# Optimization experiments

Measured on AMD Instinct MI355X. Metric: run time of the kernel, lower is better.

## Reference

```python
import jax, jax.numpy as jnp
import numpy as np

DIM = 128
BATCH = 1024


def _init_linear(key, fan_in, fan_out):
    kw, kb = jax.random.split(key)
    bound = 1.0 / np.sqrt(fan_in)
    W = jax.random.uniform(kw, (fan_in, fan_out), jnp.float32, -bound, bound)
    b = jax.random.uniform(kb, (fan_out,), jnp.float32, -bound, bound)
    return W, b


def setup_inputs() -> dict:
    key = jax.random.key(0)
    kx, ky, k1, k2, k3, k4 = jax.random.split(key, 6)
    x = jax.random.normal(kx, (BATCH, DIM), jnp.float32)
    y = jax.random.normal(ky, (BATCH, DIM), jnp.float32)
    W1, b1 = _init_linear(k1, 2 * DIM, 128)
    W2, b2 = _init_linear(k2, 128, 64)
    W3, b3 = _init_linear(k3, 64, 8)
    W4, b4 = _init_linear(k4, 8, 1)
    return {"x": x, "y": y, "W1": W1, "b1": b1, "W2": W2, "b2": b2,
            "W3": W3, "b3": b3, "W4": W4, "b4": b4}


def reference(x, y, W1, b1, W2, b2, W3, b3, W4, b4):
    # Original: pairs[i, j] = concat(x[j], y[i]); scores -> [B, B]; return transpose,
    # i.e. out[a, b] = f(concat(x[a], y[b])).
    # Split first linear algebraically: concat(x, y) @ W1 = x @ W1[:d] + y @ W1[d:].
    d = x.shape[1]
    xa = x @ W1[:d]          # [B, 128]
    yb = y @ W1[d:]          # [B, 128]
    h = jax.nn.relu(xa[:, None, :] + yb[None, :, :] + b1)  # [B, B, 128]
    h = jax.nn.relu(h @ W2 + b2)                            # [B, B, 64]
    h = jax.nn.relu(h @ W3 + b3)                            # [B, B, 8]
    out = (h @ W4 + b4)[..., 0]                             # [B, B]
    return out
```

## Files before the change

### kernel.cpp

```cpp
#include <hip/hip_runtime.h>
#include <hip/hip_bf16.h>

typedef float f32x4 __attribute__((ext_vector_type(4)));
typedef float f32x16 __attribute__((ext_vector_type(16)));
typedef short s16x8 __attribute__((ext_vector_type(8)));
typedef unsigned int u32x4 __attribute__((ext_vector_type(4)));

__device__ __forceinline__ short f2bf(float v) {
    __hip_bfloat16 h = __float2bfloat16(v);
    return __builtin_bit_cast(short, h);
}
__device__ __forceinline__ unsigned cvtpk(float lo, float hi) {
    unsigned r;
    asm("v_cvt_pk_bf16_f32 %0, %1, %2" : "=v"(r) : "v"(lo), "v"(hi));
    return r;
}
__device__ __forceinline__ void swap32(unsigned &x, unsigned &y) {
    asm("v_permlane32_swap_b32 %0, %1" : "+v"(x), "+v"(y));
}

__global__ __launch_bounds__(128) void precompute_kernel(
    const float* __restrict__ x, const float* __restrict__ y,
    const float* __restrict__ W1, const float* __restrict__ b1,
    float* __restrict__ xa, float* __restrict__ yb)
{
    __shared__ float rows[8][128];
    const int bid = blockIdx.x;
    const int k = threadIdx.x;
    const bool is_x = bid < 128;
    const int r0 = (is_x ? bid : bid - 128) * 8;
    const float* src = (is_x ? x : y) + (size_t)r0 * 128;
    const float* w = is_x ? W1 : (W1 + 128 * 128);
#pragma unroll
    for (int r = 0; r < 8; ++r) rows[r][k] = src[r * 128 + k];
    __syncthreads();
    float acc[8];
    const float bias = is_x ? b1[k] : 0.0f;
#pragma unroll
    for (int r = 0; r < 8; ++r) acc[r] = bias;
    for (int d = 0; d < 128; ++d) {
        float wv = w[d * 128 + k];
#pragma unroll
        for (int r = 0; r < 8; ++r) acc[r] = fmaf(rows[r][d], wv, acc[r]);
    }
    float* dst = (is_x ? xa : yb) + (size_t)r0 * 128 + k;
#pragma unroll
    for (int r = 0; r < 8; ++r) dst[r * 128] = acc[r];
}

__global__ __launch_bounds__(256, 2) void fused_kernel(
    const float* __restrict__ xa, const float* __restrict__ yb,
    const float* __restrict__ W2, const float* __restrict__ b2,
    const float* __restrict__ W3, const float* __restrict__ b3,
    const float* __restrict__ W4, const float* __restrict__ b4,
    float* __restrict__ out)
{
    __shared__ float xa_lds[16 * 128];

    const int tid = threadIdx.x;
    const int bid = blockIdx.x;
    const int a_chunk = bid >> 3;
    const int bq = bid & 7;
    const int wave = tid >> 6;
    const int lane = tid & 63;
    const int half = lane >> 5;
    const int m = lane & 31;
    const int bg = bq * 4 + wave;

    {
        const f32x4* xsrc = (const f32x4*)(xa + (size_t)a_chunk * 16 * 128);
        f32x4* dst = (f32x4*)xa_lds;
        dst[tid] = xsrc[tid];
        dst[tid + 256] = xsrc[tid + 256];
    }

    f32x4 yv0[8], yv1[8];
    {
        const float* yrow = yb + (size_t)(bg * 32 + m) * 128 + half * 8;
#pragma unroll
        for (int s = 0; s < 8; ++s) {
            yv0[s] = *(const f32x4*)&yrow[s * 16];
            yv1[s] = *(const f32x4*)&yrow[s * 16 + 4];
        }
    }

    s16x8 W2a[2][8];
#pragma unroll
    for (int mt = 0; mt < 2; ++mt)
#pragma unroll
        for (int s = 0; s < 8; ++s)
#pragma unroll
            for (int j = 0; j < 8; ++j)
                W2a[mt][s][j] = f2bf(W2[(s * 16 + half * 8 + j) * 64 + mt * 32 + m]);

    s16x8 W3a[4];
#pragma unroll
    for (int s = 0; s < 4; ++s)
#pragma unroll
        for (int j = 0; j < 8; ++j)
            W3a[s][j] = (m < 8) ? f2bf(W3[(s * 16 + half * 8 + j) * 8 + m]) : (short)0;

    f32x16 b2v0, b2v1, c3init;
#pragma unroll
    for (int r = 0; r < 16; ++r) {
        int f = (r & 3) + 8 * (r >> 2) + 4 * half;
        b2v0[r] = b2[f];
        b2v1[r] = b2[f + 32];
        c3init[r] = (r < 4) ? b3[(r & 3) + 4 * half] : 0.0f;
    }
    float w4v[4];
#pragma unroll
    for (int j = 0; j < 4; ++j) w4v[j] = W4[j + 4 * half];
    const float b4s = b4[0];

    __syncthreads();

    float* outp = out + (size_t)(a_chunk * 16) * 1024 + bg * 32 + m;

    for (int ai = 0; ai < 16; ++ai) {
        const float* xr = &xa_lds[ai * 128 + half * 8];
        f32x16 c20, c21;
#pragma unroll
        for (int s = 0; s < 8; ++s) {
            f32x4 x0 = *(const f32x4*)&xr[s * 16];
            f32x4 x1 = *(const f32x4*)&xr[s * 16 + 4];
            f32x4 h0 = x0 + yv0[s];
            f32x4 h1 = x1 + yv1[s];
            u32x4 q;
            q.x = cvtpk(fmaxf(h0.x, 0.f), fmaxf(h0.y, 0.f));
            q.y = cvtpk(fmaxf(h0.z, 0.f), fmaxf(h0.w, 0.f));
            q.z = cvtpk(fmaxf(h1.x, 0.f), fmaxf(h1.y, 0.f));
            q.w = cvtpk(fmaxf(h1.z, 0.f), fmaxf(h1.w, 0.f));
            s16x8 bfrag = __builtin_bit_cast(s16x8, q);
            if (s == 0) {
                c20 = __builtin_amdgcn_mfma_f32_32x32x16_bf16(W2a[0][0], bfrag, b2v0, 0, 0, 0);
                c21 = __builtin_amdgcn_mfma_f32_32x32x16_bf16(W2a[1][0], bfrag, b2v1, 0, 0, 0);
            } else {
                c20 = __builtin_amdgcn_mfma_f32_32x32x16_bf16(W2a[0][s], bfrag, c20, 0, 0, 0);
                c21 = __builtin_amdgcn_mfma_f32_32x32x16_bf16(W2a[1][s], bfrag, c21, 0, 0, 0);
            }
        }

        unsigned P[8], Q[8];
#pragma unroll
        for (int i = 0; i < 8; ++i) {
            P[i] = cvtpk(fmaxf(c20[2 * i], 0.f), fmaxf(c20[2 * i + 1], 0.f));
            Q[i] = cvtpk(fmaxf(c21[2 * i], 0.f), fmaxf(c21[2 * i + 1], 0.f));
        }
        s16x8 bf3[4];
        {
            unsigned w0 = P[0], w2 = P[2]; swap32(w0, w2);
            unsigned w1 = P[1], w3 = P[3]; swap32(w1, w3);
            u32x4 t; t.x = w0; t.y = w1; t.z = w2; t.w = w3;
            bf3[0] = __builtin_bit_cast(s16x8, t);
            unsigned v0 = P[4], v2 = P[6]; swap32(v0, v2);
            unsigned v1 = P[5], v3 = P[7]; swap32(v1, v3);
            u32x4 u; u.x = v0; u.y = v1; u.z = v2; u.w = v3;
            bf3[1] = __builtin_bit_cast(s16x8, u);
            unsigned a0 = Q[0], a2 = Q[2]; swap32(a0, a2);
            unsigned a1 = Q[1], a3 = Q[3]; swap32(a1, a3);
            u32x4 t2; t2.x = a0; t2.y = a1; t2.z = a2; t2.w = a3;
            bf3[2] = __builtin_bit_cast(s16x8, t2);
            unsigned e0 = Q[4], e2 = Q[6]; swap32(e0, e2);
            unsigned e1 = Q[5], e3 = Q[7]; swap32(e1, e3);
            u32x4 u2; u2.x = e0; u2.y = e1; u2.z = e2; u2.w = e3;
            bf3[3] = __builtin_bit_cast(s16x8, u2);
        }

        f32x16 c3 = __builtin_amdgcn_mfma_f32_32x32x16_bf16(W3a[0], bf3[0], c3init, 0, 0, 0);
#pragma unroll
        for (int s = 1; s < 4; ++s)
            c3 = __builtin_amdgcn_mfma_f32_32x32x16_bf16(W3a[s], bf3[s], c3, 0, 0, 0);

        float p = fmaxf(c3[0], 0.f) * w4v[0] + fmaxf(c3[1], 0.f) * w4v[1]
                + fmaxf(c3[2], 0.f) * w4v[2] + fmaxf(c3[3], 0.f) * w4v[3];
        unsigned pu = __builtin_bit_cast(unsigned, p);
        unsigned pv = pu;
        asm("" : "+v"(pv));
        swap32(pu, pv);
        float r = __builtin_bit_cast(float, pu) + __builtin_bit_cast(float, pv) + b4s;
        if (half == 0)
            outp[(size_t)ai * 1024] = r;
    }
}

extern "C" void kernel_launch(void* const* d_in, const int* in_sizes, int n_in,
                              void* d_out, int out_size, void* d_ws, size_t ws_size,
                              hipStream_t stream) {
    const float* x  = (const float*)d_in[0];
    const float* y  = (const float*)d_in[1];
    const float* W1 = (const float*)d_in[2];
    const float* b1 = (const float*)d_in[3];
    const float* W2 = (const float*)d_in[4];
    const float* b2 = (const float*)d_in[5];
    const float* W3 = (const float*)d_in[6];
    const float* b3 = (const float*)d_in[7];
    const float* W4 = (const float*)d_in[8];
    const float* b4 = (const float*)d_in[9];
    float* out = (float*)d_out;

    float* xa = (float*)d_ws;
    float* yb = xa + 1024 * 128;

    precompute_kernel<<<dim3(256), dim3(128), 0, stream>>>(x, y, W1, b1, xa, yb);
    fused_kernel<<<dim3(512), dim3(256), 0, stream>>>(xa, yb, W2, b2, W3, b3, W4, b4, out);
}
```

Baseline: 43.10 us.

## Stage W2/W3 bf16 fragments and biases in LDS, double grid and occupancy

New measurement: 41.61 us. 1.04x faster.

```diff
diff --git a/kernel.cpp b/kernel.cpp
--- a/kernel.cpp
+++ b/kernel.cpp
@@ -6,10 +6,6 @@
 typedef short s16x8 __attribute__((ext_vector_type(8)));
 typedef unsigned int u32x4 __attribute__((ext_vector_type(4)));
 
-__device__ __forceinline__ short f2bf(float v) {
-    __hip_bfloat16 h = __float2bfloat16(v);
-    return __builtin_bit_cast(short, h);
-}
 __device__ __forceinline__ unsigned cvtpk(float lo, float hi) {
     unsigned r;
     asm("v_cvt_pk_bf16_f32 %0, %1, %2" : "=v"(r) : "v"(lo), "v"(hi));
@@ -48,14 +44,18 @@
     for (int r = 0; r < 8; ++r) dst[r * 128] = acc[r];
 }
 
-__global__ __launch_bounds__(256, 2) void fused_kernel(
+__global__ __launch_bounds__(256, 3) void fused_kernel(
     const float* __restrict__ xa, const float* __restrict__ yb,
     const float* __restrict__ W2, const float* __restrict__ b2,
     const float* __restrict__ W3, const float* __restrict__ b3,
     const float* __restrict__ W4, const float* __restrict__ b4,
     float* __restrict__ out)
 {
-    __shared__ float xa_lds[16 * 128];
+    __shared__ float xa_lds[8 * 128];
+    __shared__ __align__(16) short w2_lds[2 * 8 * 64 * 8];
+    __shared__ __align__(16) short w3_lds[4 * 64 * 8];
+    __shared__ __align__(64) float b2_lds[64];
+    __shared__ __align__(64) float b3_lds[32];
 
     const int tid = threadIdx.x;
     const int bid = blockIdx.x;
@@ -68,11 +68,38 @@
     const int bg = bq * 4 + wave;
 
     {
-        const f32x4* xsrc = (const f32x4*)(xa + (size_t)a_chunk * 16 * 128);
-        f32x4* dst = (f32x4*)xa_lds;
-        dst[tid] = xsrc[tid];
-        dst[tid + 256] = xsrc[tid + 256];
-    }
+        const f32x4* xsrc = (const f32x4*)(xa + (size_t)a_chunk * 8 * 128);
+        ((f32x4*)xa_lds)[tid] = xsrc[tid];
+    }
+#pragma unroll
+    for (int k = 0; k < 4; ++k) {
+        int e = tid + 256 * k;
+        int l = e & 63, s = (e >> 6) & 7, mt = e >> 9;
+        int col = mt * 32 + (l & 31);
+        int krow = s * 16 + (l >> 5) * 8;
+        u32x4 q;
+#pragma unroll
+        for (int jj = 0; jj < 4; ++jj)
+            q[jj] = cvtpk(W2[(krow + 2 * jj) * 64 + col], W2[(krow + 2 * jj + 1) * 64 + col]);
+        *(u32x4*)&w2_lds[e * 8] = q;
+    }
+    {
+        int l = tid & 63, s = tid >> 6;
+        int row = l & 31;
+        int krow = s * 16 + (l >> 5) * 8;
+        u32x4 q;
+#pragma unroll
+        for (int jj = 0; jj < 4; ++jj) {
+            float lo = (row < 8) ? W3[(krow + 2 * jj) * 8 + row] : 0.f;
+            float hi = (row < 8) ? W3[(krow + 2 * jj + 1) * 8 + row] : 0.f;
+            q[jj] = cvtpk(lo, hi);
+        }
+        *(u32x4*)&w3_lds[tid * 8] = q;
+    }
+    if (tid < 64)
+        b2_lds[tid] = b2[(tid & 3) + 8 * ((tid >> 2) & 3) + 4 * ((tid >> 4) & 1) + 32 * (tid >> 5)];
+    if (tid < 32)
+        b3_lds[tid] = ((tid & 15) < 4) ? b3[(tid & 3) + 4 * (tid >> 4)] : 0.f;
 
     f32x4 yv0[8], yv1[8];
     {
@@ -83,31 +110,6 @@
             yv1[s] = *(const f32x4*)&yrow[s * 16 + 4];
         }
     }
-
-    s16x8 W2a[2][8];
-#pragma unroll
-    for (int mt = 0; mt < 2; ++mt)
-#pragma unroll
-        for (int s = 0; s < 8; ++s)
-#pragma unroll
-            for (int j = 0; j < 8; ++j)
-                W2a[mt][s][j] = f2bf(W2[(s * 16 + half * 8 + j) * 64 + mt * 32 + m]);
-
-    s16x8 W3a[4];
-#pragma unroll
-    for (int s = 0; s < 4; ++s)
-#pragma unroll
-        for (int j = 0; j < 8; ++j)
-            W3a[s][j] = (m < 8) ? f2bf(W3[(s * 16 + half * 8 + j) * 8 + m]) : (short)0;
-
-    f32x16 b2v0, b2v1, c3init;
-#pragma unroll
-    for (int r = 0; r < 16; ++r) {
-        int f = (r & 3) + 8 * (r >> 2) + 4 * half;
-        b2v0[r] = b2[f];
-        b2v1[r] = b2[f + 32];
-        c3init[r] = (r < 4) ? b3[(r & 3) + 4 * half] : 0.0f;
-    }
     float w4v[4];
 #pragma unroll
     for (int j = 0; j < 4; ++j) w4v[j] = W4[j + 4 * half];
@@ -115,9 +117,11 @@
 
     __syncthreads();
 
-    float* outp = out + (size_t)(a_chunk * 16) * 1024 + bg * 32 + m;
-
-    for (int ai = 0; ai < 16; ++ai) {
+    const short* w2p = &w2_lds[lane * 8];
+    const short* w3p = &w3_lds[lane * 8];
+    float* outp = out + (size_t)(a_chunk * 8) * 1024 + bg * 32 + m;
+
+    for (int ai = 0; ai < 8; ++ai) {
         const float* xr = &xa_lds[ai * 128 + half * 8];
         f32x16 c20, c21;
 #pragma unroll
@@ -132,12 +136,16 @@
             q.z = cvtpk(fmaxf(h1.x, 0.f), fmaxf(h1.y, 0.f));
             q.w = cvtpk(fmaxf(h1.z, 0.f), fmaxf(h1.w, 0.f));
             s16x8 bfrag = __builtin_bit_cast(s16x8, q);
+            s16x8 wf0 = *(const s16x8*)(w2p + s * 512);
+            s16x8 wf1 = *(const s16x8*)(w2p + (8 + s) * 512);
             if (s == 0) {
-                c20 = __builtin_amdgcn_mfma_f32_32x32x16_bf16(W2a[0][0], bfrag, b2v0, 0, 0, 0);
-                c21 = __builtin_amdgcn_mfma_f32_32x32x16_bf16(W2a[1][0], bfrag, b2v1, 0, 0, 0);
+                c20 = __builtin_amdgcn_mfma_f32_32x32x16_bf16(
+                    wf0, bfrag, *(const f32x16*)&b2_lds[half * 16], 0, 0, 0);
+                c21 = __builtin_amdgcn_mfma_f32_32x32x16_bf16(
+                    wf1, bfrag, *(const f32x16*)&b2_lds[32 + half * 16], 0, 0, 0);
             } else {
-                c20 = __builtin_amdgcn_mfma_f32_32x32x16_bf16(W2a[0][s], bfrag, c20, 0, 0, 0);
-                c21 = __builtin_amdgcn_mfma_f32_32x32x16_bf16(W2a[1][s], bfrag, c21, 0, 0, 0);
+                c20 = __builtin_amdgcn_mfma_f32_32x32x16_bf16(wf0, bfrag, c20, 0, 0, 0);
+                c21 = __builtin_amdgcn_mfma_f32_32x32x16_bf16(wf1, bfrag, c21, 0, 0, 0);
             }
         }
 
@@ -167,10 +175,13 @@
             bf3[3] = __builtin_bit_cast(s16x8, u2);
         }
 
-        f32x16 c3 = __builtin_amdgcn_mfma_f32_32x32x16_bf16(W3a[0], bf3[0], c3init, 0, 0, 0);
+        f32x16 c3 = __builtin_amdgcn_mfma_f32_32x32x16_bf16(
+            *(const s16x8*)(w3p + 0 * 512), bf3[0],
+            *(const f32x16*)&b3_lds[half * 16], 0, 0, 0);
 #pragma unroll
         for (int s = 1; s < 4; ++s)
-            c3 = __builtin_amdgcn_mfma_f32_32x32x16_bf16(W3a[s], bf3[s], c3, 0, 0, 0);
+            c3 = __builtin_amdgcn_mfma_f32_32x32x16_bf16(
+                *(const s16x8*)(w3p + s * 512), bf3[s], c3, 0, 0, 0);
 
         float p = fmaxf(c3[0], 0.f) * w4v[0] + fmaxf(c3[1], 0.f) * w4v[1]
                 + fmaxf(c3[2], 0.f) * w4v[2] + fmaxf(c3[3], 0.f) * w4v[3];
@@ -203,5 +214,5 @@
     float* yb = xa + 1024 * 128;
 
     precompute_kernel<<<dim3(256), dim3(128), 0, stream>>>(x, y, W1, b1, xa, yb);
-    fused_kernel<<<dim3(512), dim3(256), 0, stream>>>(xa, yb, W2, b2, W3, b3, W4, b4, out);
-}
+    fused_kernel<<<dim3(1024), dim3(256), 0, stream>>>(xa, yb, W2, b2, W3, b3, W4, b4, out);
+}
```

## Software-pipeline layer-2 fragment construction across rows with double buffers

Applied to the files above, without the earlier changes.

After: 49.69 us. +15.3%, slower.

```diff
diff --git a/kernel.cpp b/kernel.cpp
--- a/kernel.cpp
+++ b/kernel.cpp
@@ -48,6 +48,76 @@
     for (int r = 0; r < 8; ++r) dst[r * 128] = acc[r];
 }
 
+#define BUILD_FRAGS(BUF, AI)                                                   \
+    {                                                                          \
+        const float* xr_ = &xa_lds[(AI) * 128 + half * 8];                     \
+        _Pragma("unroll")                                                      \
+        for (int s_ = 0; s_ < 8; ++s_) {                                       \
+            f32x4 x0_ = *(const f32x4*)&xr_[s_ * 16];                          \
+            f32x4 x1_ = *(const f32x4*)&xr_[s_ * 16 + 4];                      \
+            f32x4 h0_ = x0_ + yv0[s_];                                         \
+            f32x4 h1_ = x1_ + yv1[s_];                                         \
+            u32x4 q_;                                                          \
+            q_.x = cvtpk(fmaxf(h0_.x, 0.f), fmaxf(h0_.y, 0.f));                \
+            q_.y = cvtpk(fmaxf(h0_.z, 0.f), fmaxf(h0_.w, 0.f));                \
+            q_.z = cvtpk(fmaxf(h1_.x, 0.f), fmaxf(h1_.y, 0.f));                \
+            q_.w = cvtpk(fmaxf(h1_.z, 0.f), fmaxf(h1_.w, 0.f));                \
+            BUF[s_] = __builtin_bit_cast(s16x8, q_);                           \
+        }                                                                      \
+    }
+
+#define PIPE_STEP(CUR, NXT, AI)                                                \
+    {                                                                          \
+        f32x16 c20 = __builtin_amdgcn_mfma_f32_32x32x16_bf16(W2a[0][0], CUR[0], b2v0, 0, 0, 0); \
+        f32x16 c21 = __builtin_amdgcn_mfma_f32_32x32x16_bf16(W2a[1][0], CUR[0], b2v1, 0, 0, 0); \
+        _Pragma("unroll")                                                      \
+        for (int s_ = 1; s_ < 8; ++s_) {                                       \
+            c20 = __builtin_amdgcn_mfma_f32_32x32x16_bf16(W2a[0][s_], CUR[s_], c20, 0, 0, 0); \
+            c21 = __builtin_amdgcn_mfma_f32_32x32x16_bf16(W2a[1][s_], CUR[s_], c21, 0, 0, 0); \
+        }                                                                      \
+        BUILD_FRAGS(NXT, ((AI) + 1) & 15)                                      \
+        unsigned P[8], Q[8];                                                   \
+        _Pragma("unroll")                                                      \
+        for (int i_ = 0; i_ < 8; ++i_) {                                       \
+            P[i_] = cvtpk(fmaxf(c20[2 * i_], 0.f), fmaxf(c20[2 * i_ + 1], 0.f)); \
+            Q[i_] = cvtpk(fmaxf(c21[2 * i_], 0.f), fmaxf(c21[2 * i_ + 1], 0.f)); \
+        }                                                                      \
+        s16x8 bf3[4];                                                          \
+        {                                                                      \
+            unsigned w0 = P[0], w2 = P[2]; swap32(w0, w2);                     \
+            unsigned w1 = P[1], w3 = P[3]; swap32(w1, w3);                     \
+            u32x4 t; t.x = w0; t.y = w1; t.z = w2; t.w = w3;                   \
+            bf3[0] = __builtin_bit_cast(s16x8, t);                             \
+            unsigned v0 = P[4], v2 = P[6]; swap32(v0, v2);                     \
+            unsigned v1 = P[5], v3 = P[7]; swap32(v1, v3);                     \
+            u32x4 u; u.x = v0; u.y = v1; u.z = v2; u.w = v3;                   \
+            bf3[1] = __builtin_bit_cast(s16x8, u);                             \
+            unsigned a0 = Q[0], a2 = Q[2]; swap32(a0, a2);                     \
+            unsigned a1 = Q[1], a3 = Q[3]; swap32(a1, a3);                     \
+            u32x4 t2; t2.x = a0; t2.y = a1; t2.z = a2; t2.w = a3;              \
+            bf3[2] = __builtin_bit_cast(s16x8, t2);                            \
+            unsigned e0 = Q[4], e2 = Q[6]; swap32(e0, e2);                     \
+            unsigned e1 = Q[5], e3 = Q[7]; swap32(e1, e3);                     \
+            u32x4 u2; u2.x = e0; u2.y = e1; u2.z = e2; u2.w = e3;              \
+            bf3[3] = __builtin_bit_cast(s16x8, u2);                            \
+        }                                                                      \
+        f32x16 c3 = __builtin_amdgcn_mfma_f32_32x32x16_bf16(W3a[0], bf3[0], fz, 0, 0, 0); \
+        _Pragma("unroll")                                                      \
+        for (int s_ = 1; s_ < 4; ++s_)                                         \
+            c3 = __builtin_amdgcn_mfma_f32_32x32x16_bf16(W3a[s_], bf3[s_], c3, 0, 0, 0); \
+        float p = 0.f;                                                         \
+        _Pragma("unroll")                                                      \
+        for (int j_ = 0; j_ < 4; ++j_)                                         \
+            p = fmaf(fmaxf(c3[j_] + b3v[j_], 0.f), w4v[j_], p);                \
+        unsigned pu = __builtin_bit_cast(unsigned, p);                         \
+        unsigned pv = pu;                                                      \
+        asm("" : "+v"(pv));                                                    \
+        swap32(pu, pv);                                                        \
+        float r_ = __builtin_bit_cast(float, pu) + __builtin_bit_cast(float, pv) + b4s; \
+        if (half == 0)                                                         \
+            outp[(size_t)(AI) * 1024] = r_;                                    \
+    }
+
 __global__ __launch_bounds__(256, 2) void fused_kernel(
     const float* __restrict__ xa, const float* __restrict__ yb,
     const float* __restrict__ W2, const float* __restrict__ b2,
@@ -100,87 +170,31 @@
         for (int j = 0; j < 8; ++j)
             W3a[s][j] = (m < 8) ? f2bf(W3[(s * 16 + half * 8 + j) * 8 + m]) : (short)0;
 
-    f32x16 b2v0, b2v1, c3init;
+    f32x16 b2v0, b2v1;
 #pragma unroll
     for (int r = 0; r < 16; ++r) {
         int f = (r & 3) + 8 * (r >> 2) + 4 * half;
         b2v0[r] = b2[f];
         b2v1[r] = b2[f + 32];
-        c3init[r] = (r < 4) ? b3[(r & 3) + 4 * half] : 0.0f;
-    }
-    float w4v[4];
-#pragma unroll
-    for (int j = 0; j < 4; ++j) w4v[j] = W4[j + 4 * half];
+    }
+    const f32x16 fz = {};
+    float b3v[4], w4v[4];
+#pragma unroll
+    for (int j = 0; j < 4; ++j) {
+        b3v[j] = b3[j + 4 * half];
+        w4v[j] = W4[j + 4 * half];
+    }
     const float b4s = b4[0];
 
     __syncthreads();
 
     float* outp = out + (size_t)(a_chunk * 16) * 1024 + bg * 32 + m;
 
-    for (int ai = 0; ai < 16; ++ai) {
-        const float* xr = &xa_lds[ai * 128 + half * 8];
-        f32x16 c20, c21;
-#pragma unroll
-        for (int s = 0; s < 8; ++s) {
-            f32x4 x0 = *(const f32x4*)&xr[s * 16];
-            f32x4 x1 = *(const f32x4*)&xr[s * 16 + 4];
-            f32x4 h0 = x0 + yv0[s];
-            f32x4 h1 = x1 + yv1[s];
-            u32x4 q;
-            q.x = cvtpk(fmaxf(h0.x, 0.f), fmaxf(h0.y, 0.f));
-            q.y = cvtpk(fmaxf(h0.z, 0.f), fmaxf(h0.w, 0.f));
-            q.z = cvtpk(fmaxf(h1.x, 0.f), fmaxf(h1.y, 0.f));
-            q.w = cvtpk(fmaxf(h1.z, 0.f), fmaxf(h1.w, 0.f));
-            s16x8 bfrag = __builtin_bit_cast(s16x8, q);
-            if (s == 0) {
-                c20 = __builtin_amdgcn_mfma_f32_32x32x16_bf16(W2a[0][0], bfrag, b2v0, 0, 0, 0);
-                c21 = __builtin_amdgcn_mfma_f32_32x32x16_bf16(W2a[1][0], bfrag, b2v1, 0, 0, 0);
-            } else {
-                c20 = __builtin_amdgcn_mfma_f32_32x32x16_bf16(W2a[0][s], bfrag, c20, 0, 0, 0);
-                c21 = __builtin_amdgcn_mfma_f32_32x32x16_bf16(W2a[1][s], bfrag, c21, 0, 0, 0);
-            }
-        }
-
-        unsigned P[8], Q[8];
-#pragma unroll
-        for (int i = 0; i < 8; ++i) {
-            P[i] = cvtpk(fmaxf(c20[2 * i], 0.f), fmaxf(c20[2 * i + 1], 0.f));
-            Q[i] = cvtpk(fmaxf(c21[2 * i], 0.f), fmaxf(c21[2 * i + 1], 0.f));
-        }
-        s16x8 bf3[4];
-        {
-            unsigned w0 = P[0], w2 = P[2]; swap32(w0, w2);
-            unsigned w1 = P[1], w3 = P[3]; swap32(w1, w3);
-            u32x4 t; t.x = w0; t.y = w1; t.z = w2; t.w = w3;
-            bf3[0] = __builtin_bit_cast(s16x8, t);
-            unsigned v0 = P[4], v2 = P[6]; swap32(v0, v2);
-            unsigned v1 = P[5], v3 = P[7]; swap32(v1, v3);
-            u32x4 u; u.x = v0; u.y = v1; u.z = v2; u.w = v3;
-            bf3[1] = __builtin_bit_cast(s16x8, u);
-            unsigned a0 = Q[0], a2 = Q[2]; swap32(a0, a2);
-            unsigned a1 = Q[1], a3 = Q[3]; swap32(a1, a3);
-            u32x4 t2; t2.x = a0; t2.y = a1; t2.z = a2; t2.w = a3;
-            bf3[2] = __builtin_bit_cast(s16x8, t2);
-            unsigned e0 = Q[4], e2 = Q[6]; swap32(e0, e2);
-            unsigned e1 = Q[5], e3 = Q[7]; swap32(e1, e3);
-            u32x4 u2; u2.x = e0; u2.y = e1; u2.z = e2; u2.w = e3;
-            bf3[3] = __builtin_bit_cast(s16x8, u2);
-        }
-
-        f32x16 c3 = __builtin_amdgcn_mfma_f32_32x32x16_bf16(W3a[0], bf3[0], c3init, 0, 0, 0);
-#pragma unroll
-        for (int s = 1; s < 4; ++s)
-            c3 = __builtin_amdgcn_mfma_f32_32x32x16_bf16(W3a[s], bf3[s], c3, 0, 0, 0);
-
-        float p = fmaxf(c3[0], 0.f) * w4v[0] + fmaxf(c3[1], 0.f) * w4v[1]
-                + fmaxf(c3[2], 0.f) * w4v[2] + fmaxf(c3[3], 0.f) * w4v[3];
-        unsigned pu = __builtin_bit_cast(unsigned, p);
-        unsigned pv = pu;
-        asm("" : "+v"(pv));
-        swap32(pu, pv);
-        float r = __builtin_bit_cast(float, pu) + __builtin_bit_cast(float, pv) + b4s;
-        if (half == 0)
-            outp[(size_t)ai * 1024] = r;
+    s16x8 bufA[8], bufB[8];
+    BUILD_FRAGS(bufA, 0)
+    for (int ai = 0; ai < 16; ai += 2) {
+        PIPE_STEP(bufA, bufB, ai)
+        PIPE_STEP(bufB, bufA, ai + 1)
     }
 }
 
```
